# Performance work log

Measured on AMD Instinct MI355X. Metric: run time of the kernel, lower is better.

Reference implementation:

```python
import jax, jax.numpy as jnp
import numpy as np
from jax import lax

BIT = 9
QMAX = float(2 ** (BIT - 1) - 1)  # 255 for 9-bit symmetric


def fake_quant(v):
    """Symmetric per-tensor 9-bit fake quantization with STE."""
    scale = jnp.max(jnp.abs(v)) / QMAX
    scale = jnp.where(scale > 0, scale, jnp.ones_like(scale))
    q = jnp.round(v / scale) * scale
    return v + lax.stop_gradient(q - v)


def qconv(x, w):
    xq = fake_quant(x)
    wq = fake_quant(w)
    return lax.conv_general_dilated(
        xq, wq, window_strides=(1, 1), padding='VALID',
        dimension_numbers=('NCHW', 'OIHW', 'NCHW'))


def qfc(x, w):
    # x: [B, Fin], w: [Fout, Fin]
    return jnp.einsum('bi,oi->bo', fake_quant(x), fake_quant(w))


def maxpool2(x):
    return lax.reduce_window(x, -jnp.inf, lax.max,
                             (1, 1, 2, 2), (1, 1, 2, 2), 'VALID')


def setup_inputs() -> dict:
    key = jax.random.key(0)
    ks = jax.random.split(key, 6)
    x = jax.random.uniform(ks[0], (4096, 3, 32, 32), dtype=jnp.float32)
    def winit(k, shape):
        fan_in = int(np.prod(shape[1:]))
        return jax.random.normal(k, shape, dtype=jnp.float32) / np.sqrt(fan_in)
    w1 = winit(ks[1], (6, 3, 5, 5))
    w2 = winit(ks[2], (16, 6, 5, 5))
    w3 = winit(ks[3], (120, 16, 5, 5))
    w4 = winit(ks[4], (84, 120))
    w5 = winit(ks[5], (10, 84))
    return {'x': x, 'w1': w1, 'w2': w2, 'w3': w3, 'w4': w4, 'w5': w5}


def reference(x, w1, w2, w3, w4, w5):
    h = maxpool2(jax.nn.relu(qconv(x, w1)))        # [B,6,14,14]
    h = maxpool2(jax.nn.relu(qconv(h, w2)))        # [B,16,5,5]
    h = jax.nn.relu(qconv(h, w3))                  # [B,120,1,1]
    h = h.reshape(h.shape[0], -1)                  # [B,120]
    h = jax.nn.relu(qfc(h, w4))                    # [B,84]
    return qfc(h, w5)                              # [B,10]
```

## Files before the change

kernel.cpp:

```cpp
#include <hip/hip_runtime.h>
#include <hip/hip_bf16.h>

#define QMAX 255.0f

typedef __attribute__((ext_vector_type(8))) short short8;
typedef __attribute__((ext_vector_type(4))) float f32x4;

#define OFF_BF1   16
#define OFF_BF2   2064
#define OFF_BF3   6160
#define OFF_BF4   32784
#define OFF_BF5   38928
#define OFF_H1    40960
#define OFF_H2    5545984
#define OFF_H3    40960
#define OFF_H4    532480

#define IMG1 3076
#define IMG2 1348

__device__ __forceinline__ float get_scale(const unsigned* slots, int i) {
    float amax = __uint_as_float(slots[i]);
    float s = amax / QMAX;
    if (!(s > 0.0f)) s = 1.0f;
    return s;
}
__device__ __forceinline__ unsigned f2bf(float f) { return __float_as_uint(f) >> 16; }

__device__ __forceinline__ float block_maxN(float v, float* red, int nw) {
    #pragma unroll
    for (int off = 32; off > 0; off >>= 1) v = fmaxf(v, __shfl_xor(v, off));
    if ((threadIdx.x & 63) == 0) red[threadIdx.x >> 6] = v;
    __syncthreads();
    float m = red[0];
    for (int i = 1; i < nw; i++) m = fmaxf(m, red[i]);
    return m;
}

__global__ __launch_bounds__(256) void k_absmax_all(
    const float4* __restrict__ x4,
    const float* __restrict__ w1, const float* __restrict__ w2,
    const float* __restrict__ w3, const float* __restrict__ w4,
    const float* __restrict__ w5, unsigned* __restrict__ slots)
{
    __shared__ float red[4];
    int b = blockIdx.x, tid = threadIdx.x;
    float m = 0.0f;
    int slot = -1;
    if (b < 2048) {
        slot = 0;
        for (int i = b * 256 + tid; i < 3145728; i += 2048 * 256) {
            float4 v = x4[i];
            m = fmaxf(m, fmaxf(fmaxf(fabsf(v.x), fabsf(v.y)), fmaxf(fabsf(v.z), fabsf(v.w))));
        }
    } else {
        int b2 = b - 2048;
        const float* w = nullptr; int n = 0, start = 0, stride = 256;
        if (b2 < 48)      { w = w3; n = 48000; start = b2 * 256;        stride = 48 * 256; slot = 7; }
        else if (b2 < 58) { w = w4; n = 10080; start = (b2 - 48) * 256; stride = 10 * 256; slot = 8; }
        else if (b2 == 58){ w = w2; n = 2400;  slot = 6; }
        else if (b2 == 59){ w = w1; n = 450;   slot = 5; }
        else if (b2 == 60){ w = w5; n = 840;   slot = 9; }
        if (slot >= 0)
            for (int i = start + tid; i < n; i += stride) m = fmaxf(m, fabsf(w[i]));
    }
    m = block_maxN(m, red, 4);
    if (tid == 0 && slot >= 0) atomicMax(&slots[slot], __float_as_uint(m));
}

__global__ __launch_bounds__(256) void k_bfrag(
    const float* __restrict__ w1, const float* __restrict__ w2,
    const float* __restrict__ w3, const float* __restrict__ w4,
    const float* __restrict__ w5, const unsigned* __restrict__ slots,
    unsigned short* __restrict__ bf1, unsigned short* __restrict__ bf2,
    unsigned short* __restrict__ bf3, unsigned short* __restrict__ bf4,
    unsigned short* __restrict__ bf5)
{
    int idx = blockIdx.x * 256 + threadIdx.x;
    if (idx < 4096) {
        int f = idx, e = f & 7, l = (f >> 3) & 63, s = (f >> 9) & 3, H = f >> 11;
        int n = l & 15, g = l >> 4, C = 4 * s + g;
        float v = 0.f;
        if (n < 12 && C < 15) {
            int o = n >> 2, dx = n & 3, kx = e - dx;
            if (kx >= 0 && kx <= 4) {
                int c = C / 5, ky = C % 5, oc = 3 * H + o;
                v = rintf(w1[((oc * 3 + c) * 5 + ky) * 5 + kx] / get_scale(slots, 5));
            }
        }
        bf1[f] = (unsigned short)f2bf(v);
    } else if (idx < 12288) {
        int f = idx - 4096, e = f & 7, l = (f >> 3) & 63, s = (f >> 9) & 7, H = f >> 12;
        int n = l & 15, g = l >> 4, C = 4 * s + g;
        float v = 0.f;
        if (C < 30) {
            int o = n >> 1, dx = n & 1, kx = e - dx;
            if (kx >= 0 && kx <= 4) {
                int c = C / 5, ky = C % 5, oc = 8 * H + o;
                v = rintf(w2[((oc * 6 + c) * 5 + ky) * 5 + kx] / get_scale(slots, 6));
            }
        }
        bf2[f] = (unsigned short)f2bf(v);
    } else if (idx < 65536) {
        int f = idx - 12288, e = f & 7, l = (f >> 3) & 63, r = f >> 9;
        int s = r % 13, Nt = r / 13;
        int oc = Nt * 16 + (l & 15), k = 32 * s + 8 * (l >> 4) + e;
        float v = 0.f;
        if (oc < 120 && k < 400) v = rintf(w3[oc * 400 + k] / get_scale(slots, 7));
        bf3[f] = (unsigned short)f2bf(v);
    } else if (idx < 77824) {
        int f = idx - 65536, e = f & 7, l = (f >> 3) & 63, r = f >> 9;
        int s = r & 3, Nt = r >> 2;
        int oc = Nt * 16 + (l & 15), k = 32 * s + 8 * (l >> 4) + e;
        float v = 0.f;
        if (oc < 84 && k < 120) v = rintf(w4[oc * 120 + k] / get_scale(slots, 8));
        bf4[f] = (unsigned short)f2bf(v);
    } else if (idx < 79360) {
        int f = idx - 77824, e = f & 7, l = (f >> 3) & 63, s = f >> 9;
        int oc = l & 15, k = 32 * s + 8 * (l >> 4) + e;
        float v = 0.f;
        if (oc < 10 && k < 84) v = rintf(w5[oc * 84 + k] / get_scale(slots, 9));
        bf5[f] = (unsigned short)f2bf(v);
    }
}

__global__ __launch_bounds__(256) void k_conv1(
    const float* __restrict__ x, const unsigned short* __restrict__ bf1,
    const unsigned* __restrict__ slots, unsigned* __restrict__ slot_out,
    float* __restrict__ h1)
{
    __shared__ unsigned short xs[4 * IMG1];
    __shared__ float red[4];
    int b0 = blockIdx.x * 4, tid = threadIdx.x;
    int lane = tid & 63, wid = tid >> 6;
    int il = lane & 15, g = lane >> 4;
    short8 Bf[2][4];
    #pragma unroll
    for (int H = 0; H < 2; H++)
        #pragma unroll
        for (int s = 0; s < 4; s++)
            Bf[H][s] = *(const short8*)(bf1 + ((H * 4 + s) * 64 + lane) * 8);
    float sx = get_scale(slots, 0);
    #pragma unroll
    for (int img = 0; img < 4; img++) {
        const float* xb = x + (long)(b0 + img) * 3072;
        for (int i = tid; i < 1536; i += 256) {
            int c = i >> 9, rem = i & 511, yy = rem >> 4, c2 = (rem & 15) << 1;
            float2 v = *(const float2*)(xb + c * 1024 + yy * 32 + c2);
            unsigned pk = f2bf(rintf(v.x / sx)) | (f2bf(rintf(v.y / sx)) << 16);
            *(unsigned*)&xs[img * IMG1 + c * 1024 + yy * 32 + c2] = pk;
        }
    }
    for (int i = tid; i < 336; i += 256) {
        int img = i / 84, rem = i % 84, c = rem / 14, py = rem % 14;
        *(float2*)(h1 + ((long)(b0 + img) * 6 + c) * 224 + py * 16 + 14) = make_float2(0.f, 0.f);
    }
    __syncthreads();
    float mscale = sx * get_scale(slots, 5);

    int abase[4];
    #pragma unroll
    for (int s = 0; s < 4; s++) {
        int C = 4 * s + g; if (C > 14) C = 14;
        abase[s] = (il >> 2) * IMG1 + (C / 5) * 1024 + (C % 5) * 32;
    }
    int q = il & 3;
    int offq = (q < 2) ? 25 * q : (q == 2 ? 50 : 74);
    int n = il, o = n >> 2, dx = n & 3;
    bool doStCol = ((n & 1) == 0) && (n < 12);
    float vmax = 0.f;
    for (int uu = wid; uu < 25; uu += 4) {
        int p = offq + uu; if (p > 97) p = 97;
        int pb = p / 14, py = p % 14;
        f32x4 acc[2][2];
        #pragma unroll
        for (int H = 0; H < 2; H++)
            #pragma unroll
            for (int yo = 0; yo < 2; yo++) acc[H][yo] = (f32x4){0.f, 0.f, 0.f, 0.f};
        #pragma unroll
        for (int yo = 0; yo < 2; yo++) {
            int y = 2 * py + yo;
            #pragma unroll
            for (int s = 0; s < 4; s++) {
                int addr = abase[s] + y * 32 + 4 * pb;
                union { unsigned long long u[2]; short8 v; } tA;
                tA.u[0] = *(const unsigned long long*)(xs + addr);
                tA.u[1] = *(const unsigned long long*)(xs + addr + 4);
                acc[0][yo] = __builtin_amdgcn_mfma_f32_16x16x32_bf16(tA.v, Bf[0][s], acc[0][yo], 0, 0, 0);
                acc[1][yo] = __builtin_amdgcn_mfma_f32_16x16x32_bf16(tA.v, Bf[1][s], acc[1][yo], 0, 0, 0);
            }
        }
        #pragma unroll
        for (int H = 0; H < 2; H++)
            #pragma unroll
            for (int r = 0; r < 4; r++) {
                float m = fmaxf(acc[H][0][r], acc[H][1][r]);
                float pooled = fmaxf(m, __shfl_xor(m, 1));
                int cntr = (r < 2) ? 25 : 24;
                if (doStCol && uu < cntr) {
                    int offr = (r < 2) ? 25 * r : (r == 2 ? 50 : 74);
                    int pr = offr + uu, pbr = pr / 14, pyr = pr % 14;
                    float v = fmaxf(pooled * mscale, 0.f);
                    int oc = 3 * H + o, px = 2 * pbr + (dx >> 1);
                    h1[((long)(b0 + g) * 6 + oc) * 224 + pyr * 16 + px] = v;
                    vmax = fmaxf(vmax, v);
                }
            }
    }
    vmax = block_maxN(vmax, red, 4);
    if (tid == 0) atomicMax(slot_out, __float_as_uint(vmax));
}

__global__ __launch_bounds__(256) void k_conv2(
    const float* __restrict__ h1, const unsigned short* __restrict__ bf2,
    const unsigned* __restrict__ slots, unsigned* __restrict__ slot_out,
    float* __restrict__ h2)
{
    __shared__ unsigned short xs[4 * IMG2];
    __shared__ float red[4];
    int b0 = blockIdx.x * 4, tid = threadIdx.x;
    int lane = tid & 63, wid = tid >> 6;
    int il = lane & 15, g = lane >> 4;
    short8 Bf[2][8];
    #pragma unroll
    for (int H = 0; H < 2; H++)
        #pragma unroll
        for (int s = 0; s < 8; s++)
            Bf[H][s] = *(const short8*)(bf2 + ((H * 8 + s) * 64 + lane) * 8);
    float s1 = get_scale(slots, 1);
    #pragma unroll
    for (int img = 0; img < 4; img++) {
        const float4* src = (const float4*)(h1 + (long)(b0 + img) * 1344);
        for (int i = tid; i < 336; i += 256) {
            float4 v = src[i];
            unsigned pk0 = f2bf(rintf(v.x / s1)) | (f2bf(rintf(v.y / s1)) << 16);
            unsigned pk1 = f2bf(rintf(v.z / s1)) | (f2bf(rintf(v.w / s1)) << 16);
            *(uint2*)&xs[img * IMG2 + 4 * i] = make_uint2(pk0, pk1);
        }
    }
    __syncthreads();
    float mscale = s1 * get_scale(slots, 6);

    int abase[8];
    #pragma unroll
    for (int s = 0; s < 8; s++) {
        int C = 4 * s + g; if (C > 29) C = 29;
        abase[s] = (il >> 2) * IMG2 + (C / 5) * 224 + (C % 5) * 16;
    }
    int q = il & 3;
    int offq = (q == 0) ? 0 : (6 * q + 1);
    int n = il, o = n >> 1;
    bool doStCol = ((n & 1) == 0);
    float vmax = 0.f;
    for (int uu = wid; uu < 7; uu += 4) {
        int p = offq + uu; if (p > 24) p = 24;
        int pb = p / 5, py = p % 5;
        f32x4 acc[2][2];
        #pragma unroll
        for (int H = 0; H < 2; H++)
            #pragma unroll
            for (int yo = 0; yo < 2; yo++) acc[H][yo] = (f32x4){0.f, 0.f, 0.f, 0.f};
        #pragma unroll
        for (int yo = 0; yo < 2; yo++) {
            int y = 2 * py + yo;
            #pragma unroll
            for (int s = 0; s < 8; s++) {
                int addr = abase[s] + y * 16 + 2 * pb;
                union { unsigned u[4]; short8 v; } tA;
                tA.u[0] = *(const unsigned*)(xs + addr);
                tA.u[1] = *(const unsigned*)(xs + addr + 2);
                tA.u[2] = *(const unsigned*)(xs + addr + 4);
                tA.u[3] = *(const unsigned*)(xs + addr + 6);
                acc[0][yo] = __builtin_amdgcn_mfma_f32_16x16x32_bf16(tA.v, Bf[0][s], acc[0][yo], 0, 0, 0);
                acc[1][yo] = __builtin_amdgcn_mfma_f32_16x16x32_bf16(tA.v, Bf[1][s], acc[1][yo], 0, 0, 0);
            }
        }
        #pragma unroll
        for (int H = 0; H < 2; H++)
            #pragma unroll
            for (int r = 0; r < 4; r++) {
                float m = fmaxf(acc[H][0][r], acc[H][1][r]);
                float pooled = fmaxf(m, __shfl_xor(m, 1));
                int cntr = (r == 0) ? 7 : 6;
                if (doStCol && uu < cntr) {
                    int offr = (r == 0) ? 0 : (6 * r + 1);
                    int pr = offr + uu, pbr = pr / 5, pyr = pr % 5;
                    float v = fmaxf(pooled * mscale, 0.f);
                    int oc = 8 * H + o;
                    h2[((long)(b0 + g) * 16 + oc) * 25 + pyr * 5 + pbr] = v;
                    vmax = fmaxf(vmax, v);
                }
            }
    }
    vmax = block_maxN(vmax, red, 4);
    if (tid == 0) atomicMax(slot_out, __float_as_uint(vmax));
}

__global__ __launch_bounds__(512) void k_conv3(
    const float* __restrict__ h2, const unsigned short* __restrict__ bf3,
    const unsigned* __restrict__ slots, unsigned* __restrict__ slot_out,
    float* __restrict__ h3)
{
    __shared__ unsigned short xs[16 * 408];
    __shared__ float red[8];
    int b0 = blockIdx.x * 16, tid = threadIdx.x;
    int lane = tid & 63, wid = tid >> 6;
    int il = lane & 15, g = lane >> 4;
    short8 Bf[13];
    #pragma unroll
    for (int s = 0; s < 13; s++)
        Bf[s] = *(const short8*)(bf3 + ((wid * 13 + s) * 64 + lane) * 8);
    float s2 = get_scale(slots, 2);
    for (int i = tid; i < 3200; i += 512) {
        int img = i / 200, p = i % 200;
        float2 v = *(const float2*)(h2 + (long)(b0 + img) * 400 + 2 * p);
        unsigned pk = f2bf(rintf(v.x / s2)) | (f2bf(rintf(v.y / s2)) << 16);
        *(unsigned*)&xs[img * 408 + 2 * p] = pk;
    }
    __syncthreads();
    float mscale = s2 * get_scale(slots, 7);
    f32x4 acc = (f32x4){0.f, 0.f, 0.f, 0.f};
    #pragma unroll
    for (int s = 0; s < 13; s++) {
        int C = 4 * s + g; if (C > 49) C = 49;
        int addr = il * 408 + 8 * C;
        union { unsigned long long u[2]; short8 v; } tA;
        tA.u[0] = *(const unsigned long long*)(xs + addr);
        tA.u[1] = *(const unsigned long long*)(xs + addr + 4);
        acc = __builtin_amdgcn_mfma_f32_16x16x32_bf16(tA.v, Bf[s], acc, 0, 0, 0);
    }
    float vmax = 0.f;
    int oc = wid * 16 + il;
    if (oc < 120) {
        #pragma unroll
        for (int r = 0; r < 4; r++) {
            float v = fmaxf(acc[r] * mscale, 0.f);
            h3[(long)(b0 + 4 * g + r) * 120 + oc] = v;
            vmax = fmaxf(vmax, v);
        }
    }
    vmax = block_maxN(vmax, red, 8);
    if (tid == 0) atomicMax(slot_out, __float_as_uint(vmax));
}

__global__ __launch_bounds__(512) void k_fc4(
    const float* __restrict__ h3, const unsigned short* __restrict__ bf4,
    const unsigned* __restrict__ slots, unsigned* __restrict__ slot_out,
    float* __restrict__ h4)
{
    __shared__ unsigned short xs[16 * 136];
    __shared__ float red[8];
    int b0 = blockIdx.x * 16, tid = threadIdx.x;
    int lane = tid & 63, wid = tid >> 6;
    int il = lane & 15, g = lane >> 4;
    short8 Bf[4];
    if (wid < 6) {
        #pragma unroll
        for (int s = 0; s < 4; s++)
            Bf[s] = *(const short8*)(bf4 + ((wid * 4 + s) * 64 + lane) * 8);
    }
    float s3 = get_scale(slots, 3);
    for (int i = tid; i < 960; i += 512) {
        int img = i / 60, p = i % 60;
        float2 v = *(const float2*)(h3 + (long)(b0 + img) * 120 + 2 * p);
        unsigned pk = f2bf(rintf(v.x / s3)) | (f2bf(rintf(v.y / s3)) << 16);
        *(unsigned*)&xs[img * 136 + 2 * p] = pk;
    }
    __syncthreads();
    float mscale = s3 * get_scale(slots, 8);
    float vmax = 0.f;
    if (wid < 6) {
        f32x4 acc = (f32x4){0.f, 0.f, 0.f, 0.f};
        #pragma unroll
        for (int s = 0; s < 4; s++) {
            int C = 4 * s + g; if (C > 14) C = 14;
            int addr = il * 136 + 8 * C;
            union { unsigned long long u[2]; short8 v; } tA;
            tA.u[0] = *(const unsigned long long*)(xs + addr);
            tA.u[1] = *(const unsigned long long*)(xs + addr + 4);
            acc = __builtin_amdgcn_mfma_f32_16x16x32_bf16(tA.v, Bf[s], acc, 0, 0, 0);
        }
        int oc = wid * 16 + il;
        if (oc < 84) {
            #pragma unroll
            for (int r = 0; r < 4; r++) {
                float v = fmaxf(acc[r] * mscale, 0.f);
                h4[(long)(b0 + 4 * g + r) * 84 + oc] = v;
                vmax = fmaxf(vmax, v);
            }
        }
    }
    vmax = block_maxN(vmax, red, 8);
    if (tid == 0) atomicMax(slot_out, __float_as_uint(vmax));
}

__global__ __launch_bounds__(256) void k_fc5(
    const float* __restrict__ h4, const unsigned short* __restrict__ bf5,
    const unsigned* __restrict__ slots, float* __restrict__ out)
{
    __shared__ unsigned short xs[4 * 16 * 104];
    int tid = threadIdx.x;
    int lane = tid & 63, w = tid >> 6;
    int il = lane & 15, g = lane >> 4;
    int b0w = blockIdx.x * 64 + w * 16;
    short8 Bf[3];
    #pragma unroll
    for (int s = 0; s < 3; s++)
        Bf[s] = *(const short8*)(bf5 + ((s * 64) + lane) * 8);
    float s4 = get_scale(slots, 4);
    for (int i = lane; i < 672; i += 64) {
        int img = i / 42, j = i % 42;
        float2 v = *(const float2*)(h4 + (long)(b0w + img) * 84 + 2 * j);
        unsigned pk = f2bf(rintf(v.x / s4)) | (f2bf(rintf(v.y / s4)) << 16);
        *(unsigned*)&xs[w * 1664 + img * 104 + 2 * j] = pk;
    }
    for (int i = lane; i < 96; i += 64) {
        int img = i / 6, j = i % 6;
        *(unsigned*)&xs[w * 1664 + img * 104 + 84 + 2 * j] = 0u;
    }
    __syncthreads();
    float mscale = s4 * get_scale(slots, 9);
    f32x4 acc = (f32x4){0.f, 0.f, 0.f, 0.f};
    #pragma unroll
    for (int s = 0; s < 3; s++) {
        int addr = w * 1664 + il * 104 + 32 * s + 8 * g;
        union { unsigned long long u[2]; short8 v; } tA;
        tA.u[0] = *(const unsigned long long*)(xs + addr);
        tA.u[1] = *(const unsigned long long*)(xs + addr + 4);
        acc = __builtin_amdgcn_mfma_f32_16x16x32_bf16(tA.v, Bf[s], acc, 0, 0, 0);
    }
    if (il < 10) {
        #pragma unroll
        for (int r = 0; r < 4; r++)
            out[(long)(b0w + 4 * g + r) * 10 + il] = acc[r] * mscale;
    }
}

extern "C" void kernel_launch(void* const* d_in, const int* in_sizes, int n_in,
                              void* d_out, int out_size, void* d_ws, size_t ws_size,
                              hipStream_t stream) {
    const float* x  = (const float*)d_in[0];
    const float* w1 = (const float*)d_in[1];
    const float* w2 = (const float*)d_in[2];
    const float* w3 = (const float*)d_in[3];
    const float* w4 = (const float*)d_in[4];
    const float* w5 = (const float*)d_in[5];
    float* out = (float*)d_out;
    float* ws = (float*)d_ws;
    unsigned* slots = (unsigned*)d_ws;
    unsigned short* bf1 = (unsigned short*)(ws + OFF_BF1);
    unsigned short* bf2 = (unsigned short*)(ws + OFF_BF2);
    unsigned short* bf3 = (unsigned short*)(ws + OFF_BF3);
    unsigned short* bf4 = (unsigned short*)(ws + OFF_BF4);
    unsigned short* bf5 = (unsigned short*)(ws + OFF_BF5);
    float* h1 = ws + OFF_H1;
    float* h2 = ws + OFF_H2;
    float* h3 = ws + OFF_H3;
    float* h4 = ws + OFF_H4;

    hipMemsetAsync(d_ws, 0, 64, stream);
    k_absmax_all<<<2112, 256, 0, stream>>>((const float4*)x, w1, w2, w3, w4, w5, slots);
    k_bfrag<<<310, 256, 0, stream>>>(w1, w2, w3, w4, w5, slots, bf1, bf2, bf3, bf4, bf5);
    k_conv1<<<1024, 256, 0, stream>>>(x, bf1, slots, slots + 1, h1);
    k_conv2<<<1024, 256, 0, stream>>>(h1, bf2, slots, slots + 2, h2);
    k_conv3<<<256, 512, 0, stream>>>(h2, bf3, slots, slots + 3, h3);
    k_fc4<<<256, 512, 0, stream>>>(h3, bf4, slots, slots + 4, h4);
    k_fc5<<<64, 256, 0, stream>>>(h4, bf5, slots, out);
}
```

Measured before the change: 119.6 us.

## Fuse conv3, fc4 and fc5 into one cooperative kernel; widen conv1 blocks

Conv3, fc4 and fc5 are merged into one cooperative kernel. Grid-wide syncs separate the stages so each global absmax scale is ready before the next layer quantizes its input. Intermediate activations stay in shared memory instead of going through global buffers, which removes two kernel launches and the h3/h4 round trips. Conv1 now handles 8 images per 512-thread block with a new output-to-lane mapping and no longer zero-fills the padding columns of h1. The costs are the grid barriers, the requirement that all blocks be co-resident, and reliance on conv2 never reading those unwritten pad columns.

```diff
diff --git a/kernel.cpp b/kernel.cpp
--- a/kernel.cpp
+++ b/kernel.cpp
@@ -1,5 +1,8 @@
 #include <hip/hip_runtime.h>
 #include <hip/hip_bf16.h>
+#include <hip/hip_cooperative_groups.h>
+
+namespace cg = cooperative_groups;
 
 #define QMAX 255.0f
 
@@ -13,15 +16,18 @@
 #define OFF_BF5   38928
 #define OFF_H1    40960
 #define OFF_H2    5545984
-#define OFF_H3    40960
-#define OFF_H4    532480
-
-#define IMG1 3076
-#define IMG2 1348
+
+#define IMG1 3080
+#define IMG2 1352
 
 __device__ __forceinline__ float get_scale(const unsigned* slots, int i) {
     float amax = __uint_as_float(slots[i]);
     float s = amax / QMAX;
+    if (!(s > 0.0f)) s = 1.0f;
+    return s;
+}
+__device__ __forceinline__ float scale_of(unsigned u) {
+    float s = __uint_as_float(u) / QMAX;
     if (!(s > 0.0f)) s = 1.0f;
     return s;
 }
@@ -124,14 +130,14 @@
     }
 }
 
-__global__ __launch_bounds__(256) void k_conv1(
+__global__ __launch_bounds__(512) void k_conv1(
     const float* __restrict__ x, const unsigned short* __restrict__ bf1,
     const unsigned* __restrict__ slots, unsigned* __restrict__ slot_out,
     float* __restrict__ h1)
 {
-    __shared__ unsigned short xs[4 * IMG1];
-    __shared__ float red[4];
-    int b0 = blockIdx.x * 4, tid = threadIdx.x;
+    __shared__ unsigned short xs[8 * IMG1];
+    __shared__ float red[8];
+    int b0 = blockIdx.x * 8, tid = threadIdx.x;
     int lane = tid & 63, wid = tid >> 6;
     int il = lane & 15, g = lane >> 4;
     short8 Bf[2][4];
@@ -142,19 +148,15 @@
             Bf[H][s] = *(const short8*)(bf1 + ((H * 4 + s) * 64 + lane) * 8);
     float sx = get_scale(slots, 0);
     #pragma unroll
-    for (int img = 0; img < 4; img++) {
+    for (int img = 0; img < 8; img++) {
         const float* xb = x + (long)(b0 + img) * 3072;
-        for (int i = tid; i < 1536; i += 256) {
+        for (int i = tid; i < 1536; i += 512) {
             int c = i >> 9, rem = i & 511, yy = rem >> 4, c2 = (rem & 15) << 1;
             float2 v = *(const float2*)(xb + c * 1024 + yy * 32 + c2);
             unsigned pk = f2bf(rintf(v.x / sx)) | (f2bf(rintf(v.y / sx)) << 16);
             *(unsigned*)&xs[img * IMG1 + c * 1024 + yy * 32 + c2] = pk;
         }
     }
-    for (int i = tid; i < 336; i += 256) {
-        int img = i / 84, rem = i % 84, c = rem / 14, py = rem % 14;
-        *(float2*)(h1 + ((long)(b0 + img) * 6 + c) * 224 + py * 16 + 14) = make_float2(0.f, 0.f);
-    }
     __syncthreads();
     float mscale = sx * get_scale(slots, 5);
 
@@ -162,16 +164,18 @@
     #pragma unroll
     for (int s = 0; s < 4; s++) {
         int C = 4 * s + g; if (C > 14) C = 14;
-        abase[s] = (il >> 2) * IMG1 + (C / 5) * 1024 + (C % 5) * 32;
-    }
-    int q = il & 3;
-    int offq = (q < 2) ? 25 * q : (q == 2 ? 50 : 74);
+        abase[s] = (il >> 1) * IMG1 + (C / 5) * 1024 + (C % 5) * 32;
+    }
+    int half = il & 1;
     int n = il, o = n >> 2, dx = n & 3;
-    bool doStCol = ((n & 1) == 0) && (n < 12);
+    bool doSt = ((n & 1) == 0) && (n < 12);
     float vmax = 0.f;
-    for (int uu = wid; uu < 25; uu += 4) {
-        int p = offq + uu; if (p > 97) p = 97;
-        int pb = p / 14, py = p % 14;
+    for (int uu = wid; uu < 49; uu += 8) {
+        int pbe = uu / 14, pye = uu - 14 * pbe;
+        int po = uu + 49;
+        int pbo = po / 14, pyo = po - 14 * pbo;
+        int pb = half ? pbo : pbe;
+        int py = half ? pyo : pye;
         f32x4 acc[2][2];
         #pragma unroll
         for (int H = 0; H < 2; H++)
@@ -196,18 +200,18 @@
             for (int r = 0; r < 4; r++) {
                 float m = fmaxf(acc[H][0][r], acc[H][1][r]);
                 float pooled = fmaxf(m, __shfl_xor(m, 1));
-                int cntr = (r < 2) ? 25 : 24;
-                if (doStCol && uu < cntr) {
-                    int offr = (r < 2) ? 25 * r : (r == 2 ? 50 : 74);
-                    int pr = offr + uu, pbr = pr / 14, pyr = pr % 14;
+                if (doSt) {
+                    int imgr = 2 * g + (r >> 1);
+                    int pbr = (r & 1) ? pbo : pbe;
+                    int pyr = (r & 1) ? pyo : pye;
                     float v = fmaxf(pooled * mscale, 0.f);
                     int oc = 3 * H + o, px = 2 * pbr + (dx >> 1);
-                    h1[((long)(b0 + g) * 6 + oc) * 224 + pyr * 16 + px] = v;
+                    h1[((long)(b0 + imgr) * 6 + oc) * 224 + pyr * 16 + px] = v;
                     vmax = fmaxf(vmax, v);
                 }
             }
     }
-    vmax = block_maxN(vmax, red, 4);
+    vmax = block_maxN(vmax, red, 8);
     if (tid == 0) atomicMax(slot_out, __float_as_uint(vmax));
 }
 
@@ -296,143 +300,144 @@
     if (tid == 0) atomicMax(slot_out, __float_as_uint(vmax));
 }
 
-__global__ __launch_bounds__(512) void k_conv3(
+__global__ __launch_bounds__(512) void k_tail(
     const float* __restrict__ h2, const unsigned short* __restrict__ bf3,
-    const unsigned* __restrict__ slots, unsigned* __restrict__ slot_out,
-    float* __restrict__ h3)
+    const unsigned short* __restrict__ bf4, const unsigned short* __restrict__ bf5,
+    unsigned* __restrict__ slots, float* __restrict__ out)
 {
     __shared__ unsigned short xs[16 * 408];
+    __shared__ float hl[16 * 124];
     __shared__ float red[8];
+    __shared__ float sh_s;
+    cg::grid_group grid = cg::this_grid();
     int b0 = blockIdx.x * 16, tid = threadIdx.x;
     int lane = tid & 63, wid = tid >> 6;
     int il = lane & 15, g = lane >> 4;
-    short8 Bf[13];
-    #pragma unroll
-    for (int s = 0; s < 13; s++)
-        Bf[s] = *(const short8*)(bf3 + ((wid * 13 + s) * 64 + lane) * 8);
-    float s2 = get_scale(slots, 2);
-    for (int i = tid; i < 3200; i += 512) {
-        int img = i / 200, p = i % 200;
-        float2 v = *(const float2*)(h2 + (long)(b0 + img) * 400 + 2 * p);
-        unsigned pk = f2bf(rintf(v.x / s2)) | (f2bf(rintf(v.y / s2)) << 16);
-        *(unsigned*)&xs[img * 408 + 2 * p] = pk;
-    }
-    __syncthreads();
-    float mscale = s2 * get_scale(slots, 7);
-    f32x4 acc = (f32x4){0.f, 0.f, 0.f, 0.f};
-    #pragma unroll
-    for (int s = 0; s < 13; s++) {
-        int C = 4 * s + g; if (C > 49) C = 49;
-        int addr = il * 408 + 8 * C;
-        union { unsigned long long u[2]; short8 v; } tA;
-        tA.u[0] = *(const unsigned long long*)(xs + addr);
-        tA.u[1] = *(const unsigned long long*)(xs + addr + 4);
-        acc = __builtin_amdgcn_mfma_f32_16x16x32_bf16(tA.v, Bf[s], acc, 0, 0, 0);
-    }
-    float vmax = 0.f;
-    int oc = wid * 16 + il;
-    if (oc < 120) {
-        #pragma unroll
-        for (int r = 0; r < 4; r++) {
-            float v = fmaxf(acc[r] * mscale, 0.f);
-            h3[(long)(b0 + 4 * g + r) * 120 + oc] = v;
-            vmax = fmaxf(vmax, v);
-        }
-    }
-    vmax = block_maxN(vmax, red, 8);
-    if (tid == 0) atomicMax(slot_out, __float_as_uint(vmax));
-}
-
-__global__ __launch_bounds__(512) void k_fc4(
-    const float* __restrict__ h3, const unsigned short* __restrict__ bf4,
-    const unsigned* __restrict__ slots, unsigned* __restrict__ slot_out,
-    float* __restrict__ h4)
-{
-    __shared__ unsigned short xs[16 * 136];
-    __shared__ float red[8];
-    int b0 = blockIdx.x * 16, tid = threadIdx.x;
-    int lane = tid & 63, wid = tid >> 6;
-    int il = lane & 15, g = lane >> 4;
-    short8 Bf[4];
-    if (wid < 6) {
-        #pragma unroll
-        for (int s = 0; s < 4; s++)
-            Bf[s] = *(const short8*)(bf4 + ((wid * 4 + s) * 64 + lane) * 8);
-    }
-    float s3 = get_scale(slots, 3);
-    for (int i = tid; i < 960; i += 512) {
-        int img = i / 60, p = i % 60;
-        float2 v = *(const float2*)(h3 + (long)(b0 + img) * 120 + 2 * p);
-        unsigned pk = f2bf(rintf(v.x / s3)) | (f2bf(rintf(v.y / s3)) << 16);
-        *(unsigned*)&xs[img * 136 + 2 * p] = pk;
-    }
-    __syncthreads();
-    float mscale = s3 * get_scale(slots, 8);
-    float vmax = 0.f;
-    if (wid < 6) {
+
+    {
+        short8 Bf[13];
+        #pragma unroll
+        for (int s = 0; s < 13; s++)
+            Bf[s] = *(const short8*)(bf3 + ((wid * 13 + s) * 64 + lane) * 8);
+        float s2 = get_scale(slots, 2);
+        for (int i = tid; i < 3200; i += 512) {
+            int img = i / 200, p = i % 200;
+            float2 v = *(const float2*)(h2 + (long)(b0 + img) * 400 + 2 * p);
+            unsigned pk = f2bf(rintf(v.x / s2)) | (f2bf(rintf(v.y / s2)) << 16);
+            *(unsigned*)&xs[img * 408 + 2 * p] = pk;
+        }
+        __syncthreads();
         f32x4 acc = (f32x4){0.f, 0.f, 0.f, 0.f};
         #pragma unroll
-        for (int s = 0; s < 4; s++) {
-            int C = 4 * s + g; if (C > 14) C = 14;
-            int addr = il * 136 + 8 * C;
+        for (int s = 0; s < 13; s++) {
+            int C = 4 * s + g; if (C > 49) C = 49;
+            int addr = il * 408 + 8 * C;
             union { unsigned long long u[2]; short8 v; } tA;
             tA.u[0] = *(const unsigned long long*)(xs + addr);
             tA.u[1] = *(const unsigned long long*)(xs + addr + 4);
             acc = __builtin_amdgcn_mfma_f32_16x16x32_bf16(tA.v, Bf[s], acc, 0, 0, 0);
         }
+        float s2w = get_scale(slots, 7);
+        float vmax = 0.f;
         int oc = wid * 16 + il;
-        if (oc < 84) {
+        __syncthreads();
+        if (oc < 120) {
+            float msc = s2 * s2w;
             #pragma unroll
             for (int r = 0; r < 4; r++) {
-                float v = fmaxf(acc[r] * mscale, 0.f);
-                h4[(long)(b0 + 4 * g + r) * 84 + oc] = v;
+                float v = fmaxf(acc[r] * msc, 0.f);
+                hl[(4 * g + r) * 124 + oc] = v;
                 vmax = fmaxf(vmax, v);
             }
         }
-    }
-    vmax = block_maxN(vmax, red, 8);
-    if (tid == 0) atomicMax(slot_out, __float_as_uint(vmax));
-}
-
-__global__ __launch_bounds__(256) void k_fc5(
-    const float* __restrict__ h4, const unsigned short* __restrict__ bf5,
-    const unsigned* __restrict__ slots, float* __restrict__ out)
-{
-    __shared__ unsigned short xs[4 * 16 * 104];
-    int tid = threadIdx.x;
-    int lane = tid & 63, w = tid >> 6;
-    int il = lane & 15, g = lane >> 4;
-    int b0w = blockIdx.x * 64 + w * 16;
-    short8 Bf[3];
-    #pragma unroll
-    for (int s = 0; s < 3; s++)
-        Bf[s] = *(const short8*)(bf5 + ((s * 64) + lane) * 8);
-    float s4 = get_scale(slots, 4);
-    for (int i = lane; i < 672; i += 64) {
-        int img = i / 42, j = i % 42;
-        float2 v = *(const float2*)(h4 + (long)(b0w + img) * 84 + 2 * j);
-        unsigned pk = f2bf(rintf(v.x / s4)) | (f2bf(rintf(v.y / s4)) << 16);
-        *(unsigned*)&xs[w * 1664 + img * 104 + 2 * j] = pk;
-    }
-    for (int i = lane; i < 96; i += 64) {
-        int img = i / 6, j = i % 6;
-        *(unsigned*)&xs[w * 1664 + img * 104 + 84 + 2 * j] = 0u;
-    }
-    __syncthreads();
-    float mscale = s4 * get_scale(slots, 9);
-    f32x4 acc = (f32x4){0.f, 0.f, 0.f, 0.f};
-    #pragma unroll
-    for (int s = 0; s < 3; s++) {
-        int addr = w * 1664 + il * 104 + 32 * s + 8 * g;
-        union { unsigned long long u[2]; short8 v; } tA;
-        tA.u[0] = *(const unsigned long long*)(xs + addr);
-        tA.u[1] = *(const unsigned long long*)(xs + addr + 4);
-        acc = __builtin_amdgcn_mfma_f32_16x16x32_bf16(tA.v, Bf[s], acc, 0, 0, 0);
-    }
-    if (il < 10) {
-        #pragma unroll
-        for (int r = 0; r < 4; r++)
-            out[(long)(b0w + 4 * g + r) * 10 + il] = acc[r] * mscale;
+        vmax = block_maxN(vmax, red, 8);
+        if (tid == 0) atomicMax(&slots[3], __float_as_uint(vmax));
+        __threadfence();
+    }
+    grid.sync();
+
+    {
+        if (tid == 0) sh_s = scale_of(atomicOr(&slots[3], 0u));
+        __syncthreads();
+        float s3 = sh_s;
+        short8 Bf[4];
+        if (wid < 6) {
+            #pragma unroll
+            for (int s = 0; s < 4; s++)
+                Bf[s] = *(const short8*)(bf4 + ((wid * 4 + s) * 64 + lane) * 8);
+        }
+        for (int i = tid; i < 960; i += 512) {
+            int img = i / 60, p = i % 60;
+            float a = hl[img * 124 + 2 * p], b = hl[img * 124 + 2 * p + 1];
+            unsigned pk = f2bf(rintf(a / s3)) | (f2bf(rintf(b / s3)) << 16);
+            *(unsigned*)&xs[img * 136 + 2 * p] = pk;
+        }
+        __syncthreads();
+        float vmax = 0.f;
+        if (wid < 6) {
+            f32x4 acc = (f32x4){0.f, 0.f, 0.f, 0.f};
+            #pragma unroll
+            for (int s = 0; s < 4; s++) {
+                int C = 4 * s + g; if (C > 14) C = 14;
+                int addr = il * 136 + 8 * C;
+                union { unsigned long long u[2]; short8 v; } tA;
+                tA.u[0] = *(const unsigned long long*)(xs + addr);
+                tA.u[1] = *(const unsigned long long*)(xs + addr + 4);
+                acc = __builtin_amdgcn_mfma_f32_16x16x32_bf16(tA.v, Bf[s], acc, 0, 0, 0);
+            }
+            int oc = wid * 16 + il;
+            float msc = s3 * get_scale(slots, 8);
+            if (oc < 84) {
+                #pragma unroll
+                for (int r = 0; r < 4; r++) {
+                    float v = fmaxf(acc[r] * msc, 0.f);
+                    hl[(4 * g + r) * 88 + oc] = v;
+                    vmax = fmaxf(vmax, v);
+                }
+            }
+        }
+        vmax = block_maxN(vmax, red, 8);
+        if (tid == 0) atomicMax(&slots[4], __float_as_uint(vmax));
+        __threadfence();
+    }
+    grid.sync();
+
+    {
+        if (tid == 0) sh_s = scale_of(atomicOr(&slots[4], 0u));
+        __syncthreads();
+        float s4 = sh_s;
+        for (int i = tid; i < 672; i += 512) {
+            int img = i / 42, j = i % 42;
+            float a = hl[img * 88 + 2 * j], b = hl[img * 88 + 2 * j + 1];
+            unsigned pk = f2bf(rintf(a / s4)) | (f2bf(rintf(b / s4)) << 16);
+            *(unsigned*)&xs[img * 104 + 2 * j] = pk;
+        }
+        for (int i = tid; i < 320; i += 512) {
+            int img = i / 20, j = i % 20;
+            xs[img * 104 + 84 + j] = 0;
+        }
+        __syncthreads();
+        if (wid == 0) {
+            short8 Bw[3];
+            #pragma unroll
+            for (int s = 0; s < 3; s++)
+                Bw[s] = *(const short8*)(bf5 + (s * 64 + lane) * 8);
+            f32x4 acc = (f32x4){0.f, 0.f, 0.f, 0.f};
+            #pragma unroll
+            for (int s = 0; s < 3; s++) {
+                int addr = il * 104 + 32 * s + 8 * g;
+                union { unsigned long long u[2]; short8 v; } tA;
+                tA.u[0] = *(const unsigned long long*)(xs + addr);
+                tA.u[1] = *(const unsigned long long*)(xs + addr + 4);
+                acc = __builtin_amdgcn_mfma_f32_16x16x32_bf16(tA.v, Bw[s], acc, 0, 0, 0);
+            }
+            if (il < 10) {
+                float msc = s4 * get_scale(slots, 9);
+                #pragma unroll
+                for (int r = 0; r < 4; r++)
+                    out[(long)(b0 + 4 * g + r) * 10 + il] = acc[r] * msc;
+            }
+        }
     }
 }
 
@@ -455,15 +460,16 @@
     unsigned short* bf5 = (unsigned short*)(ws + OFF_BF5);
     float* h1 = ws + OFF_H1;
     float* h2 = ws + OFF_H2;
-    float* h3 = ws + OFF_H3;
-    float* h4 = ws + OFF_H4;
 
     hipMemsetAsync(d_ws, 0, 64, stream);
     k_absmax_all<<<2112, 256, 0, stream>>>((const float4*)x, w1, w2, w3, w4, w5, slots);
     k_bfrag<<<310, 256, 0, stream>>>(w1, w2, w3, w4, w5, slots, bf1, bf2, bf3, bf4, bf5);
-    k_conv1<<<1024, 256, 0, stream>>>(x, bf1, slots, slots + 1, h1);
+    k_conv1<<<512, 512, 0, stream>>>(x, bf1, slots, slots + 1, h1);
     k_conv2<<<1024, 256, 0, stream>>>(h1, bf2, slots, slots + 2, h2);
-    k_conv3<<<256, 512, 0, stream>>>(h2, bf3, slots, slots + 3, h3);
-    k_fc4<<<256, 512, 0, stream>>>(h3, bf4, slots, slots + 4, h4);
-    k_fc5<<<64, 256, 0, stream>>>(h4, bf5, slots, out);
-}
+    {
+        const float* h2c = h2;
+        void* kargs[] = { (void*)&h2c, (void*)&bf3, (void*)&bf4, (void*)&bf5,
+                          (void*)&slots, (void*)&out };
+        hipLaunchCooperativeKernel((void*)k_tail, dim3(256), dim3(512), kargs, 0, stream);
+    }
+}
```

After: 223.1 us. +86.5%, slower.
